# Kernel optimization log

Hardware: AMD Instinct MI355X
Metric: run time of the kernel (lower is better)

Reference implementation:

```python
import jax, jax.numpy as jnp
from jax import lax
import numpy as np

H = 64  # hidden size

def lstm_layer(x, w_ih, w_hh, b_ih, b_hh):
    # x: [B,T,I]; w_ih: [4H,I]; w_hh: [4H,H]; gates ordered i,f,g,o (PyTorch)
    B = x.shape[0]
    xg = jnp.einsum('bti,gi->btg', x, w_ih) + b_ih  # precompute input projections [B,T,4H]
    h0 = jnp.zeros((B, H), x.dtype)
    c0 = jnp.zeros((B, H), x.dtype)
    def step(carry, xt):
        h, c = carry
        gates = xt + h @ w_hh.T + b_hh
        i, f, g, o = jnp.split(gates, 4, axis=-1)
        c = jax.nn.sigmoid(f) * c + jax.nn.sigmoid(i) * jnp.tanh(g)
        h = jax.nn.sigmoid(o) * jnp.tanh(c)
        return (h, c), h
    (hT, cT), hs = lax.scan(step, (h0, c0), jnp.swapaxes(xg, 0, 1))
    return jnp.swapaxes(hs, 0, 1), hT, cT

def layernorm(x, g, b, eps=1e-5):
    mu = jnp.mean(x, axis=-1, keepdims=True)
    var = jnp.mean(jnp.square(x - mu), axis=-1, keepdims=True)
    return (x - mu) * lax.rsqrt(var + eps) * g + b

def setup_inputs() -> dict:
    key = jax.random.key(0)
    ks = jax.random.split(key, 16)
    s = 0.05
    return {
        'x': jax.random.normal(ks[0], (512, 1024, 32), jnp.float32),
        'w_ih1': jax.random.normal(ks[1], (4 * H, 32)) * s,
        'w_hh1': jax.random.normal(ks[2], (4 * H, H)) * s,
        'b_ih1': jax.random.normal(ks[3], (4 * H,)) * s,
        'b_hh1': jax.random.normal(ks[4], (4 * H,)) * s,
        'w_ih2': jax.random.normal(ks[5], (4 * H, H)) * s,
        'w_hh2': jax.random.normal(ks[6], (4 * H, H)) * s,
        'b_ih2': jax.random.normal(ks[7], (4 * H,)) * s,
        'b_hh2': jax.random.normal(ks[8], (4 * H,)) * s,
        'fc1_w': jax.random.normal(ks[9], (128, H)) * s,
        'fc1_b': jax.random.normal(ks[10], (128,)) * s,
        'fc2_w': jax.random.normal(ks[11], (128, 128)) * s,
        'fc2_b': jax.random.normal(ks[12], (128,)) * s,
        'ln_g': jnp.ones((128,), jnp.float32),
        'ln_b': jnp.zeros((128,), jnp.float32),
    }

def reference(x, w_ih1, w_hh1, b_ih1, b_hh1, w_ih2, w_hh2, b_ih2, b_hh2,
              fc1_w, fc1_b, fc2_w, fc2_b, ln_g, ln_b):
    h1, _, _ = lstm_layer(x, w_ih1, w_hh1, b_ih1, b_hh1)
    # dropout(0.1) is identity in eval mode
    _, hT, _ = lstm_layer(h1, w_ih2, w_hh2, b_ih2, b_hh2)
    y = jax.nn.relu(hT @ fc1_w.T + fc1_b)
    y = y @ fc2_w.T + fc2_b
    return layernorm(y, ln_g, ln_b)
```

## Files before the change

### kernel.cpp

```cpp
#include <hip/hip_runtime.h>
#include <cstdint>
#include <cstddef>

#define T_STEPS 1024
#define SEG     8
#define NSEG    (T_STEPS / SEG)
#define NBLK    256
#define LOG2E   1.4426950408889634f

typedef __attribute__((ext_vector_type(8))) _Float16 half8;
typedef __attribute__((ext_vector_type(4))) float    f32x4;
typedef __attribute__((ext_vector_type(4))) int      i32x4;

static __device__ __forceinline__ float fexp2(float x) {
#if defined(__has_builtin) && __has_builtin(__builtin_amdgcn_exp2f)
  return __builtin_amdgcn_exp2f(x);
#else
  return __exp2f(x);
#endif
}
static __device__ __forceinline__ float sigm2(float a) {
  return __builtin_amdgcn_rcpf(1.0f + fexp2(-a));
}
static __device__ __forceinline__ float tanhg2(float a) {
  return 2.0f * __builtin_amdgcn_rcpf(1.0f + fexp2(-(a + a))) - 1.0f;
}
static __device__ __forceinline__ float tanhc(float c) {
  return 1.0f - 2.0f * __builtin_amdgcn_rcpf(1.0f + fexp2(c * (2.0f * LOG2E)));
}

static __device__ __forceinline__ half8 load8s(const float* s, float sc) {
  float4 a = ((const float4*)s)[0];
  float4 b = ((const float4*)s)[1];
  half8 h;
  h[0] = (_Float16)(a.x * sc); h[1] = (_Float16)(a.y * sc);
  h[2] = (_Float16)(a.z * sc); h[3] = (_Float16)(a.w * sc);
  h[4] = (_Float16)(b.x * sc); h[5] = (_Float16)(b.y * sc);
  h[6] = (_Float16)(b.z * sc); h[7] = (_Float16)(b.w * sc);
  return h;
}
static __device__ __forceinline__ i32x4 quant16(const float* src, float s) {
  union { i32x4 v; signed char b[16]; } u;
  #pragma unroll
  for (int j = 0; j < 16; ++j) u.b[j] = (signed char)__float2int_rn(src[j] * s);
  return u.v;
}

static __device__ __forceinline__ void barrier_lds() {
  __asm__ volatile("s_waitcnt lgkmcnt(0)\n\ts_barrier" ::: "memory");
}

__global__ __launch_bounds__(512, 2) void lstm_fused(
    const float* __restrict__ x,
    const float* __restrict__ w_ih1, const float* __restrict__ w_hh1,
    const float* __restrict__ b_ih1, const float* __restrict__ b_hh1,
    const float* __restrict__ w_ih2, const float* __restrict__ w_hh2,
    const float* __restrict__ b_ih2, const float* __restrict__ b_hh2,
    const float* __restrict__ fc1_w, const float* __restrict__ fc1_b,
    const float* __restrict__ fc2_w, const float* __restrict__ fc2_b,
    const float* __restrict__ ln_g, const float* __restrict__ ln_b,
    float* __restrict__ out)
{
  __shared__ __align__(16) signed char h1ring[32][2][64];
  __shared__ __align__(16) signed char h2ring[2][2][64];
  __shared__ __align__(16) float xg1b[2][SEG][2][64][4];
  __shared__ __align__(16) float xg2b[2][SEG][2][64][4];
  __shared__ __align__(16) float hfin[2][64];
  __shared__ __align__(16) float y1s[2][128];
  __shared__ __align__(16) float y2s[2][128];
  __shared__ float redmu[2], redrs[2];

  const int t   = threadIdx.x;
  const int blk = blockIdx.x;
  const int l   = t & 63;
  const int w   = t >> 6;
  const int col = l & 15;
  const int q   = l >> 4;
  const int myb = w & 1;
  const int kbase = (w & 1) * 2;

  ((int*)h1ring)[t]       = 0;
  ((int*)h1ring)[t + 512] = 0;
  if (t < 64) ((int*)h2ring)[t] = 0;

  const i32x4 zi = (i32x4){0, 0, 0, 0};
  f32x4 zf; zf[0] = 0.f; zf[1] = 0.f; zf[2] = 0.f; zf[3] = 0.f;

  i32x4 wq[4][4];
  i32x4 wq2[4][2];
  half8 wbx[4][2];
  f32x4 fsa;
  float fsx[4][2];
  float bL[4][2];

  if (w < 4) {
    const float* W = (w < 2) ? w_hh1 : w_hh2;
    float fsq[4][4];
    #pragma unroll
    for (int g = 0; g < 4; ++g) {
      #pragma unroll
      for (int k = 0; k < 4; ++k) {
        const int r = g * 64 + k * 16 + col;
        const float* p = W + r * 64 + q * 16;
        float m = 0.0f;
        #pragma unroll
        for (int j = 0; j < 16; ++j) m = fmaxf(m, fabsf(p[j]));
        m = fmaxf(m, __shfl_xor(m, 16, 64));
        m = fmaxf(m, __shfl_xor(m, 32, 64));
        wq[g][k] = quant16(p, 127.0f / m);
        fsq[g][k] = m * (LOG2E / 16129.0f);
      }
    }
    #pragma unroll
    for (int g = 0; g < 4; ++g) {
      const float v01 = (q & 1) ? fsq[g][1] : fsq[g][0];
      const float v23 = (q & 1) ? fsq[g][3] : fsq[g][2];
      fsa[g] = (q & 2) ? v23 : v01;
    }
  } else if (w < 6) {
    #pragma unroll
    for (int g = 0; g < 4; ++g) {
      #pragma unroll
      for (int k2 = 0; k2 < 2; ++k2) {
        const int r = g * 64 + (kbase + k2) * 16 + col;
        const float* p = w_ih2 + r * 64 + q * 16;
        float m = 0.0f;
        #pragma unroll
        for (int j = 0; j < 16; ++j) m = fmaxf(m, fabsf(p[j]));
        m = fmaxf(m, __shfl_xor(m, 16, 64));
        m = fmaxf(m, __shfl_xor(m, 32, 64));
        wq2[g][k2] = quant16(p, 127.0f / m);
        fsx[g][k2] = m * (LOG2E / 16129.0f);
        bL[g][k2]  = (b_ih2[r] + b_hh2[r]) * LOG2E;
      }
    }
  } else {
    #pragma unroll
    for (int g = 0; g < 4; ++g) {
      #pragma unroll
      for (int k2 = 0; k2 < 2; ++k2) {
        const int r = g * 64 + (kbase + k2) * 16 + col;
        wbx[g][k2] = load8s(w_ih1 + r * 32 + q * 8, LOG2E);
        bL[g][k2]  = (b_ih1[r] + b_hh1[r]) * LOG2E;
      }
    }
  }

  const int tl  = (l & 15) >> 1;
  const int axb = l & 1;

  float c = 0.0f;

  auto produce_xg1 = [&](int tau) {
    const float* xs = x + ((size_t)(2 * blk + axb) * T_STEPS + (tau * SEG + tl)) * 32 + q * 8;
    const float4 va = ((const float4*)xs)[0];
    const float4 vb = ((const float4*)xs)[1];
    half8 xf;
    xf[0] = (_Float16)va.x; xf[1] = (_Float16)va.y;
    xf[2] = (_Float16)va.z; xf[3] = (_Float16)va.w;
    xf[4] = (_Float16)vb.x; xf[5] = (_Float16)vb.y;
    xf[6] = (_Float16)vb.z; xf[7] = (_Float16)vb.w;
    f32x4 accf[4][2];
    #pragma unroll
    for (int g = 0; g < 4; ++g)
      #pragma unroll
      for (int k2 = 0; k2 < 2; ++k2)
        accf[g][k2] = __builtin_amdgcn_mfma_f32_16x16x32_f16(xf, wbx[g][k2], zf, 0, 0, 0);
    float* dst = &xg1b[tau & 1][0][0][0][0];
    #pragma unroll
    for (int k2 = 0; k2 < 2; ++k2) {
      #pragma unroll
      for (int r = 0; r < 4; ++r) {
        const int row = q * 4 + r;
        f32x4 v;
        v[0] = accf[0][k2][r] + bL[0][k2];
        v[1] = accf[1][k2][r] + bL[1][k2];
        v[2] = accf[2][k2][r] + bL[2][k2];
        v[3] = accf[3][k2][r] + bL[3][k2];
        *(f32x4*)(dst + (size_t)(row * 64 + (kbase + k2) * 16 + col) * 4) = v;
      }
    }
  };

  auto produce_xg2 = [&](int sg) {
    const i32x4 a = *(const i32x4*)((const signed char*)h1ring +
                    (size_t)((((sg * SEG + tl) & 31) * 128) + axb * 64 + q * 16));
    i32x4 acc[4][2];
    #pragma unroll
    for (int g = 0; g < 4; ++g)
      #pragma unroll
      for (int k2 = 0; k2 < 2; ++k2)
        acc[g][k2] = __builtin_amdgcn_mfma_i32_16x16x64_i8(a, wq2[g][k2], zi, 0, 0, 0);
    float* dst = &xg2b[sg & 1][0][0][0][0];
    #pragma unroll
    for (int k2 = 0; k2 < 2; ++k2) {
      #pragma unroll
      for (int r = 0; r < 4; ++r) {
        const int row = q * 4 + r;
        f32x4 v;
        v[0] = bL[0][k2] + fsx[0][k2] * (float)acc[0][k2][r];
        v[1] = bL[1][k2] + fsx[1][k2] * (float)acc[1][k2][r];
        v[2] = bL[2][k2] + fsx[2][k2] * (float)acc[2][k2][r];
        v[3] = bL[3][k2] + fsx[3][k2] * (float)acc[3][k2][r];
        *(f32x4*)(dst + (size_t)(row * 64 + (kbase + k2) * 16 + col) * 4) = v;
      }
    }
  };

  auto run_seg = [&](const float* XG, signed char* RING, int RM, int t0, int isl2) {
    __builtin_amdgcn_s_setprio(1);
    #pragma unroll
    for (int j8 = 0; j8 < SEG; ++j8) {
      const int tt = t0 + j8;
      const i32x4 a = *(const i32x4*)(RING + ((tt - 1) & RM) * 128 + myb * 64 + q * 16);
      const f32x4 xv = *(const f32x4*)(XG + (size_t)((j8 * 2 + myb) * 64 + l) * 4);
      i32x4 acc[4][4];
      #pragma unroll
      for (int g = 0; g < 4; ++g)
        #pragma unroll
        for (int k = 0; k < 4; ++k)
          acc[g][k] = __builtin_amdgcn_mfma_i32_16x16x64_i8(a, wq[g][k], zi, 0, 0, 0);
      float p[4];
      #pragma unroll
      for (int g = 0; g < 4; ++g) {
        const int v01 = (q & 1) ? acc[g][1][0] : acc[g][0][0];
        const int v23 = (q & 1) ? acc[g][3][0] : acc[g][2][0];
        const int ai  = (q & 2) ? v23 : v01;
        p[g] = xv[g] + fsa[g] * (float)ai;
      }
      const float gi = sigm2(p[0]), gf = sigm2(p[1]);
      const float gg = tanhg2(p[2]), go = sigm2(p[3]);
      c = gf * c + gi * gg;
      const float hv = go * tanhc(c);
      RING[(tt & RM) * 128 + myb * 64 + l] = (signed char)__float2int_rn(hv * 127.0f);
      if (isl2 && tt == T_STEPS - 1) hfin[myb][l] = hv;
    }
    __builtin_amdgcn_s_setprio(0);
  };

  if (w >= 6) produce_xg1(0);
  barrier_lds();

  for (int s = 0; s <= NSEG + 1; ++s) {
    if (w < 2) {
      if (s < NSEG)
        run_seg(&xg1b[s & 1][0][0][0][0], (signed char*)h1ring, 31, s * SEG, 0);
    } else if (w < 4) {
      const int sg = s - 2;
      if (sg >= 0)
        run_seg(&xg2b[sg & 1][0][0][0][0], (signed char*)h2ring, 1, sg * SEG, 1);
    } else if (w < 6) {
      const int sg = s - 1;
      if (sg >= 0 && sg < NSEG) produce_xg2(sg);
    } else {
      if (s + 1 < NSEG) produce_xg1(s + 1);
    }
    barrier_lds();
  }

  __syncthreads();

  if (t < 256) {
    const int bi = t >> 7, j = t & 127;
    float accv = fc1_b[j];
    const float4* w4 = (const float4*)(fc1_w + j * 64);
    const float4* h4 = (const float4*)hfin[bi];
    #pragma unroll
    for (int qq = 0; qq < 16; ++qq) {
      float4 wv = w4[qq]; float4 hv = h4[qq];
      accv += wv.x * hv.x + wv.y * hv.y + wv.z * hv.z + wv.w * hv.w;
    }
    y1s[bi][j] = fmaxf(accv, 0.0f);
  }
  __syncthreads();
  if (t < 256) {
    const int bi = t >> 7, j = t & 127;
    float accv = fc2_b[j];
    const float4* w4 = (const float4*)(fc2_w + j * 128);
    const float4* y4 = (const float4*)y1s[bi];
    #pragma unroll
    for (int qq = 0; qq < 32; ++qq) {
      float4 wv = w4[qq]; float4 yv = y4[qq];
      accv += wv.x * yv.x + wv.y * yv.y + wv.z * yv.z + wv.w * yv.w;
    }
    y2s[bi][j] = accv;
  }
  __syncthreads();
  if (t < 128) {
    const int bi = t >> 6, jj = t & 63;
    float s  = y2s[bi][jj] + y2s[bi][64 + jj];
    float qs = y2s[bi][jj] * y2s[bi][jj] + y2s[bi][64 + jj] * y2s[bi][64 + jj];
    #pragma unroll
    for (int off = 32; off > 0; off >>= 1) {
      s  += __shfl_down(s, off, 64);
      qs += __shfl_down(qs, off, 64);
    }
    if (jj == 0) {
      const float mu  = s * (1.0f / 128.0f);
      const float var = qs * (1.0f / 128.0f) - mu * mu;
      redmu[bi] = mu;
      redrs[bi] = rsqrtf(var + 1e-5f);
    }
  }
  __syncthreads();
  if (t < 256) {
    const int bi = t >> 7, j = t & 127;
    out[(size_t)(2 * blk + bi) * 128 + j] =
        (y2s[bi][j] - redmu[bi]) * redrs[bi] * ln_g[j] + ln_b[j];
  }
}

extern "C" void kernel_launch(void* const* d_in, const int* in_sizes, int n_in,
                              void* d_out, int out_size, void* d_ws, size_t ws_size,
                              hipStream_t stream) {
  const float* x     = (const float*)d_in[0];
  const float* w_ih1 = (const float*)d_in[1];
  const float* w_hh1 = (const float*)d_in[2];
  const float* b_ih1 = (const float*)d_in[3];
  const float* b_hh1 = (const float*)d_in[4];
  const float* w_ih2 = (const float*)d_in[5];
  const float* w_hh2 = (const float*)d_in[6];
  const float* b_ih2 = (const float*)d_in[7];
  const float* b_hh2 = (const float*)d_in[8];
  const float* fc1_w = (const float*)d_in[9];
  const float* fc1_b = (const float*)d_in[10];
  const float* fc2_w = (const float*)d_in[11];
  const float* fc2_b = (const float*)d_in[12];
  const float* ln_g  = (const float*)d_in[13];
  const float* ln_b  = (const float*)d_in[14];
  float* out = (float*)d_out;

  lstm_fused<<<NBLK, 512, 0, stream>>>(x, w_ih1, w_hh1, b_ih1, b_hh1,
                                       w_ih2, w_hh2, b_ih2, b_hh2,
                                       fc1_w, fc1_b, fc2_w, fc2_b,
                                       ln_g, ln_b, out);
}
```

Baseline: 409.7 us.

## Use one batch row per block and pass the LSTM hidden state through DPP registers

Each block now handles one batch element with 256 threads (4 waves), and the grid doubles to 512 blocks. Each recurrent wave owns a whole sequence and no longer goes through the LDS ring. The int8 hidden state is rebuilt into the MFMA A-operand with DPP lane shuffles, which takes the LDS store, barrier wait and reload off the serial per-step critical path. Producer waves now fill 16-step double buffers every other segment, and each segment's input-gate values are loaded up front. In exchange, each step pays a chain of DPP moves and selects, and the change relies on the DPP broadcast pattern correctly reconstructing the 16x64 A layout.

```diff
diff --git a/kernel.cpp b/kernel.cpp
--- a/kernel.cpp
+++ b/kernel.cpp
@@ -5,7 +5,8 @@
 #define T_STEPS 1024
 #define SEG     8
 #define NSEG    (T_STEPS / SEG)
-#define NBLK    256
+#define NPAIR   (NSEG / 2)
+#define NBLK    512
 #define LOG2E   1.4426950408889634f
 
 typedef __attribute__((ext_vector_type(8))) _Float16 half8;
@@ -50,7 +51,7 @@
   __asm__ volatile("s_waitcnt lgkmcnt(0)\n\ts_barrier" ::: "memory");
 }
 
-__global__ __launch_bounds__(512, 2) void lstm_fused(
+__global__ __launch_bounds__(256, 2) void lstm_fused(
     const float* __restrict__ x,
     const float* __restrict__ w_ih1, const float* __restrict__ w_hh1,
     const float* __restrict__ b_ih1, const float* __restrict__ b_hh1,
@@ -61,14 +62,13 @@
     const float* __restrict__ ln_g, const float* __restrict__ ln_b,
     float* __restrict__ out)
 {
-  __shared__ __align__(16) signed char h1ring[32][2][64];
-  __shared__ __align__(16) signed char h2ring[2][2][64];
-  __shared__ __align__(16) float xg1b[2][SEG][2][64][4];
-  __shared__ __align__(16) float xg2b[2][SEG][2][64][4];
-  __shared__ __align__(16) float hfin[2][64];
-  __shared__ __align__(16) float y1s[2][128];
-  __shared__ __align__(16) float y2s[2][128];
-  __shared__ float redmu[2], redrs[2];
+  __shared__ __align__(16) signed char h1ring[32][64];
+  __shared__ __align__(16) float xg1b[2][16][64][4];
+  __shared__ __align__(16) float xg2b[2][16][64][4];
+  __shared__ __align__(16) float hfin[64];
+  __shared__ __align__(16) float y1s[128];
+  __shared__ __align__(16) float y2s[128];
+  __shared__ float redmu, redrs;
 
   const int t   = threadIdx.x;
   const int blk = blockIdx.x;
@@ -76,25 +76,18 @@
   const int w   = t >> 6;
   const int col = l & 15;
   const int q   = l >> 4;
-  const int myb = w & 1;
-  const int kbase = (w & 1) * 2;
-
-  ((int*)h1ring)[t]       = 0;
-  ((int*)h1ring)[t + 512] = 0;
-  if (t < 64) ((int*)h2ring)[t] = 0;
 
   const i32x4 zi = (i32x4){0, 0, 0, 0};
   f32x4 zf; zf[0] = 0.f; zf[1] = 0.f; zf[2] = 0.f; zf[3] = 0.f;
 
   i32x4 wq[4][4];
-  i32x4 wq2[4][2];
-  half8 wbx[4][2];
+  half8 wbx[4][4];
   f32x4 fsa;
-  float fsx[4][2];
-  float bL[4][2];
-
-  if (w < 4) {
-    const float* W = (w < 2) ? w_hh1 : w_hh2;
+  float fsx[4][4];
+  float bL[4][4];
+
+  if (w < 2) {
+    const float* W = w ? w_hh2 : w_hh1;
     float fsq[4][4];
     #pragma unroll
     for (int g = 0; g < 4; ++g) {
@@ -117,42 +110,46 @@
       const float v23 = (q & 1) ? fsq[g][3] : fsq[g][2];
       fsa[g] = (q & 2) ? v23 : v01;
     }
-  } else if (w < 6) {
+  } else if (w == 2) {
     #pragma unroll
     for (int g = 0; g < 4; ++g) {
       #pragma unroll
-      for (int k2 = 0; k2 < 2; ++k2) {
-        const int r = g * 64 + (kbase + k2) * 16 + col;
+      for (int k = 0; k < 4; ++k) {
+        const int r = g * 64 + k * 16 + col;
         const float* p = w_ih2 + r * 64 + q * 16;
         float m = 0.0f;
         #pragma unroll
         for (int j = 0; j < 16; ++j) m = fmaxf(m, fabsf(p[j]));
         m = fmaxf(m, __shfl_xor(m, 16, 64));
         m = fmaxf(m, __shfl_xor(m, 32, 64));
-        wq2[g][k2] = quant16(p, 127.0f / m);
-        fsx[g][k2] = m * (LOG2E / 16129.0f);
-        bL[g][k2]  = (b_ih2[r] + b_hh2[r]) * LOG2E;
+        wq[g][k] = quant16(p, 127.0f / m);
+        fsx[g][k] = m * (LOG2E / 16129.0f);
+        bL[g][k]  = (b_ih2[r] + b_hh2[r]) * LOG2E;
       }
     }
   } else {
     #pragma unroll
     for (int g = 0; g < 4; ++g) {
       #pragma unroll
-      for (int k2 = 0; k2 < 2; ++k2) {
-        const int r = g * 64 + (kbase + k2) * 16 + col;
-        wbx[g][k2] = load8s(w_ih1 + r * 32 + q * 8, LOG2E);
-        bL[g][k2]  = (b_ih1[r] + b_hh1[r]) * LOG2E;
-      }
-    }
-  }
-
-  const int tl  = (l & 15) >> 1;
-  const int axb = l & 1;
-
-  float c = 0.0f;
-
-  auto produce_xg1 = [&](int tau) {
-    const float* xs = x + ((size_t)(2 * blk + axb) * T_STEPS + (tau * SEG + tl)) * 32 + q * 8;
+      for (int k = 0; k < 4; ++k) {
+        const int r = g * 64 + k * 16 + col;
+        wbx[g][k] = load8s(w_ih1 + r * 32 + q * 8, LOG2E);
+        bL[g][k]  = (b_ih1[r] + b_hh1[r]) * LOG2E;
+      }
+    }
+  }
+
+  float c  = 0.0f;
+  i32x4 af = zi;
+  const int sh1 = (l & 1) << 3;
+  const int sh2 = (l & 2) << 3;
+  const int jb0 = (l >> 2) & 1;
+  const int jb1 = (l >> 2) & 2;
+
+  const int tl = l & 15;
+
+  auto produce_xg1 = [&](int P) {
+    const float* xs = x + ((size_t)blk * T_STEPS + (P * 16 + tl)) * 32 + q * 8;
     const float4 va = ((const float4*)xs)[0];
     const float4 vb = ((const float4*)xs)[1];
     half8 xf;
@@ -160,153 +157,172 @@
     xf[2] = (_Float16)va.z; xf[3] = (_Float16)va.w;
     xf[4] = (_Float16)vb.x; xf[5] = (_Float16)vb.y;
     xf[6] = (_Float16)vb.z; xf[7] = (_Float16)vb.w;
-    f32x4 accf[4][2];
+    f32x4 accf[4][4];
     #pragma unroll
     for (int g = 0; g < 4; ++g)
       #pragma unroll
-      for (int k2 = 0; k2 < 2; ++k2)
-        accf[g][k2] = __builtin_amdgcn_mfma_f32_16x16x32_f16(xf, wbx[g][k2], zf, 0, 0, 0);
-    float* dst = &xg1b[tau & 1][0][0][0][0];
-    #pragma unroll
-    for (int k2 = 0; k2 < 2; ++k2) {
+      for (int k = 0; k < 4; ++k)
+        accf[g][k] = __builtin_amdgcn_mfma_f32_16x16x32_f16(xf, wbx[g][k], zf, 0, 0, 0);
+    float* dst = &xg1b[P & 1][0][0][0];
+    #pragma unroll
+    for (int k = 0; k < 4; ++k) {
       #pragma unroll
       for (int r = 0; r < 4; ++r) {
         const int row = q * 4 + r;
         f32x4 v;
-        v[0] = accf[0][k2][r] + bL[0][k2];
-        v[1] = accf[1][k2][r] + bL[1][k2];
-        v[2] = accf[2][k2][r] + bL[2][k2];
-        v[3] = accf[3][k2][r] + bL[3][k2];
-        *(f32x4*)(dst + (size_t)(row * 64 + (kbase + k2) * 16 + col) * 4) = v;
+        v[0] = accf[0][k][r] + bL[0][k];
+        v[1] = accf[1][k][r] + bL[1][k];
+        v[2] = accf[2][k][r] + bL[2][k];
+        v[3] = accf[3][k][r] + bL[3][k];
+        *(f32x4*)(dst + (size_t)(row * 64 + k * 16 + col) * 4) = v;
       }
     }
   };
 
-  auto produce_xg2 = [&](int sg) {
-    const i32x4 a = *(const i32x4*)((const signed char*)h1ring +
-                    (size_t)((((sg * SEG + tl) & 31) * 128) + axb * 64 + q * 16));
-    i32x4 acc[4][2];
+  auto produce_xg2 = [&](int P) {
+    const i32x4 a = *(const i32x4*)&h1ring[(P * 16 + tl) & 31][q * 16];
+    i32x4 acc[4][4];
     #pragma unroll
     for (int g = 0; g < 4; ++g)
       #pragma unroll
-      for (int k2 = 0; k2 < 2; ++k2)
-        acc[g][k2] = __builtin_amdgcn_mfma_i32_16x16x64_i8(a, wq2[g][k2], zi, 0, 0, 0);
-    float* dst = &xg2b[sg & 1][0][0][0][0];
-    #pragma unroll
-    for (int k2 = 0; k2 < 2; ++k2) {
+      for (int k = 0; k < 4; ++k)
+        acc[g][k] = __builtin_amdgcn_mfma_i32_16x16x64_i8(a, wq[g][k], zi, 0, 0, 0);
+    float* dst = &xg2b[P & 1][0][0][0];
+    #pragma unroll
+    for (int k = 0; k < 4; ++k) {
       #pragma unroll
       for (int r = 0; r < 4; ++r) {
         const int row = q * 4 + r;
         f32x4 v;
-        v[0] = bL[0][k2] + fsx[0][k2] * (float)acc[0][k2][r];
-        v[1] = bL[1][k2] + fsx[1][k2] * (float)acc[1][k2][r];
-        v[2] = bL[2][k2] + fsx[2][k2] * (float)acc[2][k2][r];
-        v[3] = bL[3][k2] + fsx[3][k2] * (float)acc[3][k2][r];
-        *(f32x4*)(dst + (size_t)(row * 64 + (kbase + k2) * 16 + col) * 4) = v;
+        v[0] = bL[0][k] + fsx[0][k] * (float)acc[0][k][r];
+        v[1] = bL[1][k] + fsx[1][k] * (float)acc[1][k][r];
+        v[2] = bL[2][k] + fsx[2][k] * (float)acc[2][k][r];
+        v[3] = bL[3][k] + fsx[3][k] * (float)acc[3][k][r];
+        *(f32x4*)(dst + (size_t)(row * 64 + k * 16 + col) * 4) = v;
       }
     }
   };
 
-  auto run_seg = [&](const float* XG, signed char* RING, int RM, int t0, int isl2) {
+  auto run_seg = [&](const float* XG, int t0, bool ring, bool fin) {
+    f32x4 xq[8];
+    #pragma unroll
+    for (int j = 0; j < 8; ++j)
+      xq[j] = *(const f32x4*)(XG + (size_t)(j * 64 + l) * 4);
     __builtin_amdgcn_s_setprio(1);
     #pragma unroll
     for (int j8 = 0; j8 < SEG; ++j8) {
-      const int tt = t0 + j8;
-      const i32x4 a = *(const i32x4*)(RING + ((tt - 1) & RM) * 128 + myb * 64 + q * 16);
-      const f32x4 xv = *(const f32x4*)(XG + (size_t)((j8 * 2 + myb) * 64 + l) * 4);
       i32x4 acc[4][4];
       #pragma unroll
       for (int g = 0; g < 4; ++g)
         #pragma unroll
         for (int k = 0; k < 4; ++k)
-          acc[g][k] = __builtin_amdgcn_mfma_i32_16x16x64_i8(a, wq[g][k], zi, 0, 0, 0);
+          acc[g][k] = __builtin_amdgcn_mfma_i32_16x16x64_i8(af, wq[g][k], zi, 0, 0, 0);
       float p[4];
       #pragma unroll
       for (int g = 0; g < 4; ++g) {
-        const int v01 = (q & 1) ? acc[g][1][0] : acc[g][0][0];
-        const int v23 = (q & 1) ? acc[g][3][0] : acc[g][2][0];
-        const int ai  = (q & 2) ? v23 : v01;
-        p[g] = xv[g] + fsa[g] * (float)ai;
+        const int a01 = (q & 1) ? acc[g][1][0] : acc[g][0][0];
+        const int a23 = (q & 1) ? acc[g][3][0] : acc[g][2][0];
+        const int ai  = (q & 2) ? a23 : a01;
+        p[g] = xq[j8][g] + fsa[g] * (float)ai;
       }
       const float gi = sigm2(p[0]), gf = sigm2(p[1]);
       const float gg = tanhg2(p[2]), go = sigm2(p[3]);
       c = gf * c + gi * gg;
       const float hv = go * tanhc(c);
-      RING[(tt & RM) * 128 + myb * 64 + l] = (signed char)__float2int_rn(hv * 127.0f);
-      if (isl2 && tt == T_STEPS - 1) hfin[myb][l] = hv;
+      const int  B  = __float2int_rn(hv * 127.0f) & 255;
+      if (ring)
+        ((unsigned char*)h1ring)[((t0 + j8) & 31) * 64 + l] = (unsigned char)B;
+      if (fin && j8 == SEG - 1) hfin[l] = hv;
+      const int a1 = B << sh1;
+      const int t1 = __builtin_amdgcn_mov_dpp(a1, 0xB1, 0xF, 0xF, false);
+      const int u  = a1 | t1;
+      const int a2 = u << sh2;
+      const int t2 = __builtin_amdgcn_mov_dpp(a2, 0x4E, 0xF, 0xF, false);
+      const int D  = a2 | t2;
+      const int e1 = __builtin_amdgcn_mov_dpp(D, 0x124, 0xF, 0xF, false);
+      const int e2 = __builtin_amdgcn_mov_dpp(D, 0x128, 0xF, 0xF, false);
+      const int e3 = __builtin_amdgcn_mov_dpp(D, 0x12C, 0xF, 0xF, false);
+      const int e0 = D;
+      const int v0 = jb1 ? (jb0 ? e3 : e2) : (jb0 ? e1 : e0);
+      const int v1 = jb1 ? (jb0 ? e2 : e1) : (jb0 ? e0 : e3);
+      const int v2 = jb1 ? (jb0 ? e1 : e0) : (jb0 ? e3 : e2);
+      const int v3 = jb1 ? (jb0 ? e0 : e3) : (jb0 ? e2 : e1);
+      af = (i32x4){v0, v1, v2, v3};
     }
     __builtin_amdgcn_s_setprio(0);
   };
 
-  if (w >= 6) produce_xg1(0);
+  if (w == 3) produce_xg1(0);
   barrier_lds();
 
-  for (int s = 0; s <= NSEG + 1; ++s) {
-    if (w < 2) {
+  for (int s = 0; s <= NSEG + 2; ++s) {
+    if (w == 0) {
       if (s < NSEG)
-        run_seg(&xg1b[s & 1][0][0][0][0], (signed char*)h1ring, 31, s * SEG, 0);
-    } else if (w < 4) {
-      const int sg = s - 2;
+        run_seg(&xg1b[(s >> 1) & 1][(s & 1) * 8][0][0], s * SEG, true, false);
+    } else if (w == 1) {
+      const int sg = s - 3;
       if (sg >= 0)
-        run_seg(&xg2b[sg & 1][0][0][0][0], (signed char*)h2ring, 1, sg * SEG, 1);
-    } else if (w < 6) {
-      const int sg = s - 1;
-      if (sg >= 0 && sg < NSEG) produce_xg2(sg);
+        run_seg(&xg2b[(sg >> 1) & 1][(sg & 1) * 8][0][0], sg * SEG, false,
+                sg == NSEG - 1);
+    } else if (w == 2) {
+      if (s >= 2 && !(s & 1)) {
+        const int P = (s - 2) >> 1;
+        if (P < NPAIR) produce_xg2(P);
+      }
     } else {
-      if (s + 1 < NSEG) produce_xg1(s + 1);
+      if (!(s & 1)) {
+        const int P = (s >> 1) + 1;
+        if (P < NPAIR) produce_xg1(P);
+      }
     }
     barrier_lds();
   }
 
   __syncthreads();
 
-  if (t < 256) {
-    const int bi = t >> 7, j = t & 127;
-    float accv = fc1_b[j];
-    const float4* w4 = (const float4*)(fc1_w + j * 64);
-    const float4* h4 = (const float4*)hfin[bi];
+  if (t < 128) {
+    float a = fc1_b[t];
+    const float4* w4 = (const float4*)(fc1_w + t * 64);
+    const float4* h4 = (const float4*)hfin;
     #pragma unroll
     for (int qq = 0; qq < 16; ++qq) {
       float4 wv = w4[qq]; float4 hv = h4[qq];
-      accv += wv.x * hv.x + wv.y * hv.y + wv.z * hv.z + wv.w * hv.w;
-    }
-    y1s[bi][j] = fmaxf(accv, 0.0f);
+      a += wv.x * hv.x + wv.y * hv.y + wv.z * hv.z + wv.w * hv.w;
+    }
+    y1s[t] = fmaxf(a, 0.0f);
   }
   __syncthreads();
-  if (t < 256) {
-    const int bi = t >> 7, j = t & 127;
-    float accv = fc2_b[j];
-    const float4* w4 = (const float4*)(fc2_w + j * 128);
-    const float4* y4 = (const float4*)y1s[bi];
+  if (t < 128) {
+    float a = fc2_b[t];
+    const float4* w4 = (const float4*)(fc2_w + t * 128);
+    const float4* y4 = (const float4*)y1s;
     #pragma unroll
     for (int qq = 0; qq < 32; ++qq) {
       float4 wv = w4[qq]; float4 yv = y4[qq];
-      accv += wv.x * yv.x + wv.y * yv.y + wv.z * yv.z + wv.w * yv.w;
-    }
-    y2s[bi][j] = accv;
+      a += wv.x * yv.x + wv.y * yv.y + wv.z * yv.z + wv.w * yv.w;
+    }
+    y2s[t] = a;
+  }
+  __syncthreads();
+  if (t < 64) {
+    float s_  = y2s[t] + y2s[64 + t];
+    float qs  = y2s[t] * y2s[t] + y2s[64 + t] * y2s[64 + t];
+    #pragma unroll
+    for (int off = 32; off > 0; off >>= 1) {
+      s_ += __shfl_down(s_, off, 64);
+      qs += __shfl_down(qs, off, 64);
+    }
+    if (t == 0) {
+      const float mu  = s_ * (1.0f / 128.0f);
+      const float var = qs * (1.0f / 128.0f) - mu * mu;
+      redmu = mu;
+      redrs = rsqrtf(var + 1e-5f);
+    }
   }
   __syncthreads();
   if (t < 128) {
-    const int bi = t >> 6, jj = t & 63;
-    float s  = y2s[bi][jj] + y2s[bi][64 + jj];
-    float qs = y2s[bi][jj] * y2s[bi][jj] + y2s[bi][64 + jj] * y2s[bi][64 + jj];
-    #pragma unroll
-    for (int off = 32; off > 0; off >>= 1) {
-      s  += __shfl_down(s, off, 64);
-      qs += __shfl_down(qs, off, 64);
-    }
-    if (jj == 0) {
-      const float mu  = s * (1.0f / 128.0f);
-      const float var = qs * (1.0f / 128.0f) - mu * mu;
-      redmu[bi] = mu;
-      redrs[bi] = rsqrtf(var + 1e-5f);
-    }
-  }
-  __syncthreads();
-  if (t < 256) {
-    const int bi = t >> 7, j = t & 127;
-    out[(size_t)(2 * blk + bi) * 128 + j] =
-        (y2s[bi][j] - redmu[bi]) * redrs[bi] * ln_g[j] + ln_b[j];
+    out[(size_t)blk * 128 + t] =
+        (y2s[t] - redmu) * redrs * ln_g[t] + ln_b[t];
   }
 }
 
@@ -330,7 +346,7 @@
   const float* ln_b  = (const float*)d_in[14];
   float* out = (float*)d_out;
 
-  lstm_fused<<<NBLK, 512, 0, stream>>>(x, w_ih1, w_hh1, b_ih1, b_hh1,
+  lstm_fused<<<NBLK, 256, 0, stream>>>(x, w_ih1, w_hh1, b_ih1, b_hh1,
                                        w_ih2, w_hh2, b_ih2, b_hh2,
                                        fc1_w, fc1_b, fc2_w, fc2_b,
                                        ln_g, ln_b, out);
```

Result: slower. 573.0 us (+39.9%).

## Keep recurrent hidden state in registers via DPP shuffles instead of LDS ring

Applied to the files above, without the earlier changes.

The recurrent wavefronts no longer write the int8 hidden state to an LDS ring and read it back each step. They now pack the bytes across lanes with DPP row shuffles and rebuild the MFMA A-operand in registers, and the layer-2 ring is removed entirely. Layer 1 still writes h1ring for the layer-2 producer. The xg loads for a whole segment are also hoisted ahead of the step loop. This removes per-step LDS latency on the serial recurrence, at the cost of extra DPP/select ALU work and register pressure.

```diff
diff --git a/kernel.cpp b/kernel.cpp
--- a/kernel.cpp
+++ b/kernel.cpp
@@ -62,7 +62,6 @@
     float* __restrict__ out)
 {
   __shared__ __align__(16) signed char h1ring[32][2][64];
-  __shared__ __align__(16) signed char h2ring[2][2][64];
   __shared__ __align__(16) float xg1b[2][SEG][2][64][4];
   __shared__ __align__(16) float xg2b[2][SEG][2][64][4];
   __shared__ __align__(16) float hfin[2][64];
@@ -81,7 +80,6 @@
 
   ((int*)h1ring)[t]       = 0;
   ((int*)h1ring)[t + 512] = 0;
-  if (t < 64) ((int*)h2ring)[t] = 0;
 
   const i32x4 zi = (i32x4){0, 0, 0, 0};
   f32x4 zf; zf[0] = 0.f; zf[1] = 0.f; zf[2] = 0.f; zf[3] = 0.f;
@@ -149,7 +147,12 @@
   const int tl  = (l & 15) >> 1;
   const int axb = l & 1;
 
-  float c = 0.0f;
+  float c  = 0.0f;
+  i32x4 af = zi;
+  const int sh1 = (l & 1) << 3;
+  const int sh2 = (l & 2) << 3;
+  const int jb0 = (l >> 2) & 1;
+  const int jb1 = (l >> 2) & 2;
 
   auto produce_xg1 = [&](int tau) {
     const float* xs = x + ((size_t)(2 * blk + axb) * T_STEPS + (tau * SEG + tl)) * 32 + q * 8;
@@ -207,33 +210,51 @@
     }
   };
 
-  auto run_seg = [&](const float* XG, signed char* RING, int RM, int t0, int isl2) {
+  auto run_seg = [&](const float* XG, int t0, bool ring, bool fin) {
+    f32x4 xq[8];
+    #pragma unroll
+    for (int j = 0; j < 8; ++j)
+      xq[j] = *(const f32x4*)(XG + (size_t)((j * 2 + myb) * 64 + l) * 4);
     __builtin_amdgcn_s_setprio(1);
     #pragma unroll
     for (int j8 = 0; j8 < SEG; ++j8) {
-      const int tt = t0 + j8;
-      const i32x4 a = *(const i32x4*)(RING + ((tt - 1) & RM) * 128 + myb * 64 + q * 16);
-      const f32x4 xv = *(const f32x4*)(XG + (size_t)((j8 * 2 + myb) * 64 + l) * 4);
       i32x4 acc[4][4];
       #pragma unroll
       for (int g = 0; g < 4; ++g)
         #pragma unroll
         for (int k = 0; k < 4; ++k)
-          acc[g][k] = __builtin_amdgcn_mfma_i32_16x16x64_i8(a, wq[g][k], zi, 0, 0, 0);
+          acc[g][k] = __builtin_amdgcn_mfma_i32_16x16x64_i8(af, wq[g][k], zi, 0, 0, 0);
       float p[4];
       #pragma unroll
       for (int g = 0; g < 4; ++g) {
-        const int v01 = (q & 1) ? acc[g][1][0] : acc[g][0][0];
-        const int v23 = (q & 1) ? acc[g][3][0] : acc[g][2][0];
-        const int ai  = (q & 2) ? v23 : v01;
-        p[g] = xv[g] + fsa[g] * (float)ai;
+        const int a01 = (q & 1) ? acc[g][1][0] : acc[g][0][0];
+        const int a23 = (q & 1) ? acc[g][3][0] : acc[g][2][0];
+        const int ai  = (q & 2) ? a23 : a01;
+        p[g] = xq[j8][g] + fsa[g] * (float)ai;
       }
       const float gi = sigm2(p[0]), gf = sigm2(p[1]);
       const float gg = tanhg2(p[2]), go = sigm2(p[3]);
       c = gf * c + gi * gg;
       const float hv = go * tanhc(c);
-      RING[(tt & RM) * 128 + myb * 64 + l] = (signed char)__float2int_rn(hv * 127.0f);
-      if (isl2 && tt == T_STEPS - 1) hfin[myb][l] = hv;
+      const int  B  = __float2int_rn(hv * 127.0f) & 255;
+      if (ring)
+        ((signed char*)h1ring)[((t0 + j8) & 31) * 128 + myb * 64 + l] = (signed char)B;
+      if (fin && j8 == SEG - 1) hfin[myb][l] = hv;
+      const int a1 = B << sh1;
+      const int t1 = __builtin_amdgcn_mov_dpp(a1, 0xB1, 0xF, 0xF, false);
+      const int u  = a1 | t1;
+      const int a2 = u << sh2;
+      const int t2 = __builtin_amdgcn_mov_dpp(a2, 0x4E, 0xF, 0xF, false);
+      const int D  = a2 | t2;
+      const int e1 = __builtin_amdgcn_mov_dpp(D, 0x124, 0xF, 0xF, false);
+      const int e2 = __builtin_amdgcn_mov_dpp(D, 0x128, 0xF, 0xF, false);
+      const int e3 = __builtin_amdgcn_mov_dpp(D, 0x12C, 0xF, 0xF, false);
+      const int e0 = D;
+      const int v0 = jb1 ? (jb0 ? e3 : e2) : (jb0 ? e1 : e0);
+      const int v1 = jb1 ? (jb0 ? e2 : e1) : (jb0 ? e0 : e3);
+      const int v2 = jb1 ? (jb0 ? e1 : e0) : (jb0 ? e3 : e2);
+      const int v3 = jb1 ? (jb0 ? e0 : e3) : (jb0 ? e2 : e1);
+      af = (i32x4){v0, v1, v2, v3};
     }
     __builtin_amdgcn_s_setprio(0);
   };
@@ -244,11 +265,11 @@
   for (int s = 0; s <= NSEG + 1; ++s) {
     if (w < 2) {
       if (s < NSEG)
-        run_seg(&xg1b[s & 1][0][0][0][0], (signed char*)h1ring, 31, s * SEG, 0);
+        run_seg(&xg1b[s & 1][0][0][0][0], s * SEG, true, false);
     } else if (w < 4) {
       const int sg = s - 2;
       if (sg >= 0)
-        run_seg(&xg2b[sg & 1][0][0][0][0], (signed char*)h2ring, 1, sg * SEG, 1);
+        run_seg(&xg2b[sg & 1][0][0][0][0], sg * SEG, false, sg == NSEG - 1);
     } else if (w < 6) {
       const int sg = s - 1;
       if (sg >= 0 && sg < NSEG) produce_xg2(sg);
```

Result: no change. 417.2 us (+1.8%).

## Double segment length and prefetch gate inputs into registers ahead of recurrence

Applied to the files above, without the earlier changes.

Segment length grows from 8 to 16 steps, which halves the number of block-wide barriers across the pipelined recurrence. Producers now compute two 8-step halves per segment. The recurrent loop preloads 8 steps of precomputed gate inputs into registers and refills them 8 steps ahead, which takes LDS reads off the serial critical path. The scale by 127 is folded into the tanh constants, and the final-hidden check is simplified; the risk is that the xg buffers and ring sizes (the 31 mask) are not shown to have grown for 16 steps.

```diff
diff --git a/kernel.cpp b/kernel.cpp
--- a/kernel.cpp
+++ b/kernel.cpp
@@ -3,7 +3,7 @@
 #include <cstddef>
 
 #define T_STEPS 1024
-#define SEG     8
+#define SEG     16
 #define NSEG    (T_STEPS / SEG)
 #define NBLK    256
 #define LOG2E   1.4426950408889634f
@@ -25,8 +25,8 @@
 static __device__ __forceinline__ float tanhg2(float a) {
   return 2.0f * __builtin_amdgcn_rcpf(1.0f + fexp2(-(a + a))) - 1.0f;
 }
-static __device__ __forceinline__ float tanhc(float c) {
-  return 1.0f - 2.0f * __builtin_amdgcn_rcpf(1.0f + fexp2(c * (2.0f * LOG2E)));
+static __device__ __forceinline__ float tanhc127(float c) {
+  return 127.0f - 254.0f * __builtin_amdgcn_rcpf(1.0f + fexp2(c * (2.0f * LOG2E)));
 }
 
 static __device__ __forceinline__ half8 load8s(const float* s, float sc) {
@@ -152,68 +152,81 @@
   float c = 0.0f;
 
   auto produce_xg1 = [&](int tau) {
-    const float* xs = x + ((size_t)(2 * blk + axb) * T_STEPS + (tau * SEG + tl)) * 32 + q * 8;
-    const float4 va = ((const float4*)xs)[0];
-    const float4 vb = ((const float4*)xs)[1];
-    half8 xf;
-    xf[0] = (_Float16)va.x; xf[1] = (_Float16)va.y;
-    xf[2] = (_Float16)va.z; xf[3] = (_Float16)va.w;
-    xf[4] = (_Float16)vb.x; xf[5] = (_Float16)vb.y;
-    xf[6] = (_Float16)vb.z; xf[7] = (_Float16)vb.w;
-    f32x4 accf[4][2];
-    #pragma unroll
-    for (int g = 0; g < 4; ++g)
-      #pragma unroll
-      for (int k2 = 0; k2 < 2; ++k2)
-        accf[g][k2] = __builtin_amdgcn_mfma_f32_16x16x32_f16(xf, wbx[g][k2], zf, 0, 0, 0);
     float* dst = &xg1b[tau & 1][0][0][0][0];
     #pragma unroll
-    for (int k2 = 0; k2 < 2; ++k2) {
-      #pragma unroll
-      for (int r = 0; r < 4; ++r) {
-        const int row = q * 4 + r;
-        f32x4 v;
-        v[0] = accf[0][k2][r] + bL[0][k2];
-        v[1] = accf[1][k2][r] + bL[1][k2];
-        v[2] = accf[2][k2][r] + bL[2][k2];
-        v[3] = accf[3][k2][r] + bL[3][k2];
-        *(f32x4*)(dst + (size_t)(row * 64 + (kbase + k2) * 16 + col) * 4) = v;
+    for (int h8 = 0; h8 < 2; ++h8) {
+      const float* xs = x + ((size_t)(2 * blk + axb) * T_STEPS +
+                             (tau * SEG + h8 * 8 + tl)) * 32 + q * 8;
+      const float4 va = ((const float4*)xs)[0];
+      const float4 vb = ((const float4*)xs)[1];
+      half8 xf;
+      xf[0] = (_Float16)va.x; xf[1] = (_Float16)va.y;
+      xf[2] = (_Float16)va.z; xf[3] = (_Float16)va.w;
+      xf[4] = (_Float16)vb.x; xf[5] = (_Float16)vb.y;
+      xf[6] = (_Float16)vb.z; xf[7] = (_Float16)vb.w;
+      f32x4 accf[4][2];
+      #pragma unroll
+      for (int g = 0; g < 4; ++g)
+        #pragma unroll
+        for (int k2 = 0; k2 < 2; ++k2)
+          accf[g][k2] = __builtin_amdgcn_mfma_f32_16x16x32_f16(xf, wbx[g][k2], zf, 0, 0, 0);
+      #pragma unroll
+      for (int k2 = 0; k2 < 2; ++k2) {
+        #pragma unroll
+        for (int r = 0; r < 4; ++r) {
+          const int row = h8 * 16 + q * 4 + r;
+          f32x4 v;
+          v[0] = accf[0][k2][r] + bL[0][k2];
+          v[1] = accf[1][k2][r] + bL[1][k2];
+          v[2] = accf[2][k2][r] + bL[2][k2];
+          v[3] = accf[3][k2][r] + bL[3][k2];
+          *(f32x4*)(dst + (size_t)(row * 64 + (kbase + k2) * 16 + col) * 4) = v;
+        }
       }
     }
   };
 
   auto produce_xg2 = [&](int sg) {
-    const i32x4 a = *(const i32x4*)((const signed char*)h1ring +
-                    (size_t)((((sg * SEG + tl) & 31) * 128) + axb * 64 + q * 16));
-    i32x4 acc[4][2];
-    #pragma unroll
-    for (int g = 0; g < 4; ++g)
-      #pragma unroll
-      for (int k2 = 0; k2 < 2; ++k2)
-        acc[g][k2] = __builtin_amdgcn_mfma_i32_16x16x64_i8(a, wq2[g][k2], zi, 0, 0, 0);
     float* dst = &xg2b[sg & 1][0][0][0][0];
     #pragma unroll
-    for (int k2 = 0; k2 < 2; ++k2) {
-      #pragma unroll
-      for (int r = 0; r < 4; ++r) {
-        const int row = q * 4 + r;
-        f32x4 v;
-        v[0] = bL[0][k2] + fsx[0][k2] * (float)acc[0][k2][r];
-        v[1] = bL[1][k2] + fsx[1][k2] * (float)acc[1][k2][r];
-        v[2] = bL[2][k2] + fsx[2][k2] * (float)acc[2][k2][r];
-        v[3] = bL[3][k2] + fsx[3][k2] * (float)acc[3][k2][r];
-        *(f32x4*)(dst + (size_t)(row * 64 + (kbase + k2) * 16 + col) * 4) = v;
+    for (int h8 = 0; h8 < 2; ++h8) {
+      const i32x4 a = *(const i32x4*)((const signed char*)h1ring +
+                      (size_t)((((sg * SEG + h8 * 8 + tl) & 31) * 128) + axb * 64 + q * 16));
+      i32x4 acc[4][2];
+      #pragma unroll
+      for (int g = 0; g < 4; ++g)
+        #pragma unroll
+        for (int k2 = 0; k2 < 2; ++k2)
+          acc[g][k2] = __builtin_amdgcn_mfma_i32_16x16x64_i8(a, wq2[g][k2], zi, 0, 0, 0);
+      #pragma unroll
+      for (int k2 = 0; k2 < 2; ++k2) {
+        #pragma unroll
+        for (int r = 0; r < 4; ++r) {
+          const int row = h8 * 16 + q * 4 + r;
+          f32x4 v;
+          v[0] = bL[0][k2] + fsx[0][k2] * (float)acc[0][k2][r];
+          v[1] = bL[1][k2] + fsx[1][k2] * (float)acc[1][k2][r];
+          v[2] = bL[2][k2] + fsx[2][k2] * (float)acc[2][k2][r];
+          v[3] = bL[3][k2] + fsx[3][k2] * (float)acc[3][k2][r];
+          *(f32x4*)(dst + (size_t)(row * 64 + (kbase + k2) * 16 + col) * 4) = v;
+        }
       }
     }
   };
 
-  auto run_seg = [&](const float* XG, signed char* RING, int RM, int t0, int isl2) {
+  auto run_seg = [&](const float* XG, signed char* RING, int RM, int t0, bool fin) {
+    f32x4 xq[8];
+    #pragma unroll
+    for (int j = 0; j < 8; ++j)
+      xq[j] = *(const f32x4*)(XG + (size_t)((j * 2 + myb) * 64 + l) * 4);
     __builtin_amdgcn_s_setprio(1);
     #pragma unroll
     for (int j8 = 0; j8 < SEG; ++j8) {
       const int tt = t0 + j8;
       const i32x4 a = *(const i32x4*)(RING + ((tt - 1) & RM) * 128 + myb * 64 + q * 16);
-      const f32x4 xv = *(const f32x4*)(XG + (size_t)((j8 * 2 + myb) * 64 + l) * 4);
+      const f32x4 xv = xq[j8 & 7];
+      if (j8 < 8)
+        xq[j8 & 7] = *(const f32x4*)(XG + (size_t)(((j8 + 8) * 2 + myb) * 64 + l) * 4);
       i32x4 acc[4][4];
       #pragma unroll
       for (int g = 0; g < 4; ++g)
@@ -223,17 +236,17 @@
       float p[4];
       #pragma unroll
       for (int g = 0; g < 4; ++g) {
-        const int v01 = (q & 1) ? acc[g][1][0] : acc[g][0][0];
-        const int v23 = (q & 1) ? acc[g][3][0] : acc[g][2][0];
-        const int ai  = (q & 2) ? v23 : v01;
+        const int a01 = (q & 1) ? acc[g][1][0] : acc[g][0][0];
+        const int a23 = (q & 1) ? acc[g][3][0] : acc[g][2][0];
+        const int ai  = (q & 2) ? a23 : a01;
         p[g] = xv[g] + fsa[g] * (float)ai;
       }
       const float gi = sigm2(p[0]), gf = sigm2(p[1]);
       const float gg = tanhg2(p[2]), go = sigm2(p[3]);
       c = gf * c + gi * gg;
-      const float hv = go * tanhc(c);
-      RING[(tt & RM) * 128 + myb * 64 + l] = (signed char)__float2int_rn(hv * 127.0f);
-      if (isl2 && tt == T_STEPS - 1) hfin[myb][l] = hv;
+      const float hq = go * tanhc127(c);
+      RING[(tt & RM) * 128 + myb * 64 + l] = (signed char)__float2int_rn(hq);
+      if (fin && j8 == SEG - 1) hfin[myb][l] = hq * (1.0f / 127.0f);
     }
     __builtin_amdgcn_s_setprio(0);
   };
@@ -244,11 +257,12 @@
   for (int s = 0; s <= NSEG + 1; ++s) {
     if (w < 2) {
       if (s < NSEG)
-        run_seg(&xg1b[s & 1][0][0][0][0], (signed char*)h1ring, 31, s * SEG, 0);
+        run_seg(&xg1b[s & 1][0][0][0][0], (signed char*)h1ring, 31, s * SEG, false);
     } else if (w < 4) {
       const int sg = s - 2;
       if (sg >= 0)
-        run_seg(&xg2b[sg & 1][0][0][0][0], (signed char*)h2ring, 1, sg * SEG, 1);
+        run_seg(&xg2b[sg & 1][0][0][0][0], (signed char*)h2ring, 1, sg * SEG,
+                sg == NSEG - 1);
     } else if (w < 6) {
       const int sg = s - 1;
       if (sg >= 0 && sg < NSEG) produce_xg2(sg);
```

Measured after the change: 409.1 us. No clear change (-0.1%).
